# Kernel tuning notes

Hardware: AMD Instinct MI355X
Metric: run time of the kernel (lower is better)

Reference implementation:

```python
import jax, jax.numpy as jnp
import numpy as np
import math

DIM, DEPTH, HEADS, VOCAB, DMODEL = 200, 6, 10, 7, 512
DH = DIM // HEADS                      # 20
NBF = int(DH * math.log(DH))           # 59 FAVOR+ random features
FF = 4 * DIM                           # 800


def setup_inputs() -> dict:
    key = jax.random.key(0)
    ks = iter(jax.random.split(key, 32))
    s = 0.02
    inp = {
        'x': jax.random.normal(next(ks), (4, 16, 2048), jnp.float32),
        'token_emb': jax.random.normal(next(ks), (VOCAB, DIM)) * s,
        'ln1_g': jnp.ones((DEPTH, DIM)), 'ln1_b': jnp.zeros((DEPTH, DIM)),
        'wq': jax.random.normal(next(ks), (DEPTH, DIM, DIM)) * s, 'bq': jnp.zeros((DEPTH, DIM)),
        'wk': jax.random.normal(next(ks), (DEPTH, DIM, DIM)) * s, 'bk': jnp.zeros((DEPTH, DIM)),
        'wv': jax.random.normal(next(ks), (DEPTH, DIM, DIM)) * s, 'bv': jnp.zeros((DEPTH, DIM)),
        'proj': jax.random.normal(next(ks), (DEPTH, NBF, DH)),  # FAVOR+ projection (buffer)
        'wo': jax.random.normal(next(ks), (DEPTH, DIM, DIM)) * s, 'bo': jnp.zeros((DEPTH, DIM)),
        'ln2_g': jnp.ones((DEPTH, DIM)), 'ln2_b': jnp.zeros((DEPTH, DIM)),
        'ffw1': jax.random.normal(next(ks), (DEPTH, DIM, FF)) * s, 'ffb1': jnp.zeros((DEPTH, FF)),
        'ffw2': jax.random.normal(next(ks), (DEPTH, FF, DIM)) * s, 'ffb2': jnp.zeros((DEPTH, DIM)),
        'lnf_g': jnp.ones((DIM,)), 'lnf_b': jnp.zeros((DIM,)),
        'proj_w': jax.random.normal(next(ks), (DIM, DMODEL)) * s, 'proj_b': jnp.zeros((DMODEL,)),
    }
    return inp


def layer_norm(x, g, b, eps=1e-5):
    mu = x.mean(-1, keepdims=True)
    var = ((x - mu) ** 2).mean(-1, keepdims=True)
    return (x - mu) / jnp.sqrt(var + eps) * g + b


def softmax_kernel(data, proj, is_query, eps=1e-4):
    # data: (N,H,S,dh); proj: (m,dh)
    dn = data * (data.shape[-1] ** -0.25)
    dash = jnp.einsum('nhsd,md->nhsm', dn, proj)
    diag = 0.5 * jnp.sum(dn * dn, axis=-1, keepdims=True)
    mx = jnp.max(dash, axis=-1, keepdims=True) if is_query else jnp.max(dash)
    return (proj.shape[0] ** -0.5) * (jnp.exp(dash - diag - mx) + eps)


def attention(x, wq, bq, wk, bk, wv, bv, proj, wo, bo):
    N, S, D = x.shape
    split = lambda t: t.reshape(N, S, HEADS, DH).transpose(0, 2, 1, 3)
    q, k, v = split(x @ wq + bq), split(x @ wk + bk), split(x @ wv + bv)
    qp = softmax_kernel(q, proj, True)
    kp = softmax_kernel(k, proj, False)
    d_inv = 1.0 / jnp.einsum('nhsm,nhm->nhs', qp, kp.sum(axis=2))
    ctx = jnp.einsum('nhsm,nhsd->nhmd', kp, v)          # linear attention context
    out = jnp.einsum('nhsm,nhmd->nhsd', qp, ctx) * d_inv[..., None]
    return out.transpose(0, 2, 1, 3).reshape(N, S, D) @ wo + bo


def feedforward(x, w1, b1, w2, b2):
    return jax.nn.gelu(x @ w1 + b1, approximate=False) @ w2 + b2


def performer_forward(tokens, p):
    h = p['token_emb'][tokens]            # pos_emb is zeros (g2v_position_emb=False)
    x1, x2 = h, h                         # reversible net: x duplicated along channels
    for l in range(DEPTH):
        x1 = x1 + attention(layer_norm(x2, p['ln1_g'][l], p['ln1_b'][l]),
                            p['wq'][l], p['bq'][l], p['wk'][l], p['bk'][l],
                            p['wv'][l], p['bv'][l], p['proj'][l], p['wo'][l], p['bo'][l])
        x2 = x2 + feedforward(layer_norm(x1, p['ln2_g'][l], p['ln2_b'][l]),
                              p['ffw1'][l], p['ffb1'][l], p['ffw2'][l], p['ffb2'][l])
    h = 0.5 * (x1 + x2)                   # mean over the two reversible halves
    return layer_norm(h, p['lnf_g'], p['lnf_b'])


def reference(x, token_emb, ln1_g, ln1_b, wq, bq, wk, bk, wv, bv, proj, wo, bo,
              ln2_g, ln2_b, ffw1, ffb1, ffw2, ffb2, lnf_g, lnf_b, proj_w, proj_b):
    p = dict(token_emb=token_emb, ln1_g=ln1_g, ln1_b=ln1_b, wq=wq, bq=bq, wk=wk, bk=bk,
             wv=wv, bv=bv, proj=proj, wo=wo, bo=bo, ln2_g=ln2_g, ln2_b=ln2_b,
             ffw1=ffw1, ffb1=ffb1, ffw2=ffw2, ffb2=ffb2, lnf_g=lnf_g, lnf_b=lnf_b)
    B, Nt, T = x.shape
    xf = x.reshape(B * Nt, T)
    # torch.quantile on 1D positives -> bin_edges shape (1,4) != (T,4), so the
    # original falls back to zero bin edges; edges_plus = [0,0,0,0,inf], hence
    # token = 4 if value > 0 else 0, then + cls_token_id (1).
    tokens = jnp.where(xf > 0, 4, 0).astype(jnp.int32) + 1
    # chunk loop (chunk_size=512 samples) is identity math: run all at once
    enc = performer_forward(tokens, p)    # (B*Nt, T, DIM)
    pooled = enc.mean(axis=1)             # mean-pool over sequence
    out = pooled @ proj_w + proj_b
    return out.reshape(B, Nt, DMODEL)
```

## Files before the change

kernel.cpp:

```cpp
#include <hip/hip_runtime.h>
#include <hip/hip_bf16.h>
#include <math.h>

#define DEPTH   6
#define DIM     200
#define HEADS   10
#define DH      20
#define NBF     59
#define FFD     800
#define DMODEL  512
#define NSEQ    64
#define SEQ     2048
#define NTOK    (NSEQ*SEQ)
#define KPAD    224
#define BUFPAD  64
#define KNROW   40
#define VROW    136
#define KPROW   136
#define QPROW   72
#define CTXR    21
#define HSROW   132
#define HSTRIDE ((size_t)NTOK * DH)
#define PKV_E   (512*KPAD)
#define PQ_E    (256*KPAD)
#define PWO_E   (256*KPAD)
#define PF1_E   (896*KPAD)
#define PF2_E   (256*800)

typedef __hip_bfloat16 bf16;
typedef unsigned short u16;
typedef short s8v __attribute__((ext_vector_type(8)));
typedef short s4v __attribute__((ext_vector_type(4)));
typedef float f4v __attribute__((ext_vector_type(4)));

constexpr float SCALE = 0.4728708045015879f;
constexpr float RATIO = 0.1301889109808239f;
constexpr float KEPS  = 1e-4f;

__device__ __forceinline__ float b2f(bf16 v) { return __bfloat162float(v); }
__device__ __forceinline__ bf16 f2b(float v) { return __float2bfloat16(v); }
__device__ __forceinline__ float bfu(u16 u) {
    return __uint_as_float(((unsigned)u) << 16);
}
__device__ __forceinline__ u16 f2u(float v) {
    bf16 hb = __float2bfloat16(v);
    return *(u16*)&hb;
}
__device__ __forceinline__ float gelu_f(float x) {
    float inner = 0.7978845608028654f * (x + 0.044715f * x * x * x);
    float e = __expf(2.f * inner);
    return x * (1.f - 1.f / (e + 1.f));
}
__device__ __forceinline__ void gld_lds16(const short* g, short* l) {
    __builtin_amdgcn_global_load_lds(
        (const __attribute__((address_space(1))) void*)g,
        (__attribute__((address_space(3))) void*)l, 16, 0, 0);
}
#define MFMA16(a, b, c) __builtin_amdgcn_mfma_f32_16x16x32_bf16(a, b, c, 0, 0, 0)

__global__ void sentinel_kernel(float* out, float wsmb) {
    if (threadIdx.x == 0) out[0] = wsmb;
}

__global__ void zeropad_kernel(bf16* p1, bf16* p2, bf16* p3, bf16* p4) {
    int i = threadIdx.x;
    if (i < BUFPAD) {
        bf16 z = f2b(0.f);
        p1[i] = z; p2[i] = z; p3[i] = z; p4[i] = z;
    }
}

__global__ __launch_bounds__(256) void prep_layer(
        const float* __restrict__ wq, const float* __restrict__ wk,
        const float* __restrict__ wv, const float* __restrict__ wo,
        const float* __restrict__ f1, const float* __restrict__ f2,
        const float* __restrict__ g1, const float* __restrict__ b1,
        const float* __restrict__ g2, const float* __restrict__ b2,
        const float* __restrict__ bq, const float* __restrict__ bk,
        const float* __restrict__ bv, const float* __restrict__ f1b,
        bf16* __restrict__ pKV, bf16* __restrict__ pQ, bf16* __restrict__ pWO,
        bf16* __restrict__ pF1, bf16* __restrict__ pF2,
        float* __restrict__ uw) {
    int b = blockIdx.x, t = threadIdx.x;
    if (b < 448) {
        int idx = b * 256 + t;
        int row = idx / KPAD, k = idx % KPAD;
        float v = 0.f;
        if (k < DIM) {
            if (row < DIM) v = wk[(size_t)k * DIM + row] * g1[k];
            else if (row >= 256 && row < 256 + DIM)
                v = wv[(size_t)k * DIM + (row - 256)] * g1[k];
        }
        pKV[idx] = f2b(v);
    } else if (b < 672) {
        int idx = (b - 448) * 256 + t;
        int row = idx / KPAD, k = idx % KPAD;
        float v = (row < DIM && k < DIM) ? wq[(size_t)k * DIM + row] * g1[k] : 0.f;
        pQ[idx] = f2b(v);
    } else if (b < 896) {
        int idx = (b - 672) * 256 + t;
        int row = idx / KPAD, k = idx % KPAD;
        float v = (row < DIM && k < DIM) ? wo[(size_t)k * DIM + row] : 0.f;
        pWO[idx] = f2b(v);
    } else if (b < 1680) {
        int idx = (b - 896) * 256 + t;
        int row = idx / KPAD, k = idx % KPAD;
        float v = (row < FFD && k < DIM) ? f1[(size_t)k * FFD + row] * g2[k] : 0.f;
        pF1[idx] = f2b(v);
    } else if (b < 2480) {
        int idx = (b - 1680) * 256 + t;
        int row = idx / 800, k = idx % 800;
        float v = (row < DIM) ? f2[(size_t)k * DIM + row] : 0.f;
        pF2[idx] = f2b(v);
    } else if (b < 2482) {
        int j = b - 2480;
        const float* W    = j ? wv : wk;
        const float* bias = j ? bv : bk;
        int n = t;
        float su = 0.f, sw = 0.f;
        if (n < DIM) {
            for (int k = 0; k < DIM; ++k) {
                float wvv = W[(size_t)k * DIM + n];
                su += g1[k] * wvv;
                sw += b1[k] * wvv;
            }
            sw += bias[n];
        }
        uw[j * 256 + n] = su;
        uw[512 + j * 256 + n] = sw;
    } else if (b == 2482) {
        int n = t;
        float su = 0.f, sw = 0.f;
        if (n < DIM) {
            for (int k = 0; k < DIM; ++k) {
                float wvv = wq[(size_t)k * DIM + n];
                su += g1[k] * wvv;
                sw += b1[k] * wvv;
            }
            sw += bq[n];
        }
        uw[1024 + n] = su;
        uw[1280 + n] = sw;
    } else {
        int n = (b - 2483) * 256 + t;
        if (n < 896) {
            float su = 0.f, sw = 0.f;
            if (n < FFD) {
                for (int k = 0; k < DIM; ++k) {
                    float wvv = f1[(size_t)k * FFD + n];
                    su += g2[k] * wvv;
                    sw += b2[k] * wvv;
                }
                sw += f1b[n];
            }
            uw[1536 + n] = su;
            uw[2432 + n] = sw;
        }
    }
}

__global__ __launch_bounds__(256) void embed_kernel(const float* __restrict__ x,
        const float* __restrict__ emb, bf16* __restrict__ x1, bf16* __restrict__ x2) {
    int idx = blockIdx.x * 256 + threadIdx.x;
    if (idx >= NTOK * 25) return;
    int t = idx / 25, c = idx % 25;
    int row = (x[t] > 0.f) ? 5 : 1;
    const float4* e4 = (const float4*)(emb + row * DIM + c * 8);
    float4 e0 = e4[0], e1 = e4[1];
    s8v o;
    o[0] = (short)f2u(e0.x); o[1] = (short)f2u(e0.y);
    o[2] = (short)f2u(e0.z); o[3] = (short)f2u(e0.w);
    o[4] = (short)f2u(e1.x); o[5] = (short)f2u(e1.y);
    o[6] = (short)f2u(e1.z); o[7] = (short)f2u(e1.w);
    size_t off = (size_t)t * DIM + c * 8;
    *(s8v*)((short*)x1 + off) = o;
    *(s8v*)((short*)x2 + off) = o;
}

__global__ __launch_bounds__(256) void lnstats_kernel(const bf16* __restrict__ in,
        float* __restrict__ mu_o, float* __restrict__ rstd_o) {
    int lane = threadIdx.x & 63;
    size_t t = (size_t)blockIdx.x * 4 + (threadIdx.x >> 6);
    const u16* row = (const u16*)in + t * DIM;
    float v0 = 0.f, v1 = 0.f, v2 = 0.f, v3 = 0.f;
    if (lane < 50) {
        ushort4 u4 = ((const ushort4*)row)[lane];
        v0 = bfu(u4.x); v1 = bfu(u4.y); v2 = bfu(u4.z); v3 = bfu(u4.w);
    }
    float s = v0 + v1 + v2 + v3, qq = v0*v0 + v1*v1 + v2*v2 + v3*v3;
    #pragma unroll
    for (int o = 32; o > 0; o >>= 1) { s += __shfl_xor(s, o); qq += __shfl_xor(qq, o); }
    if (lane == 0) {
        float mu = s * (1.f / DIM);
        mu_o[t] = mu;
        rstd_o[t] = rsqrtf(qq * (1.f / DIM) - mu * mu + 1e-5f);
    }
}

__global__ __launch_bounds__(256) void finalln_kernel(const bf16* __restrict__ in1,
        const bf16* __restrict__ in2, const float* __restrict__ g,
        const float* __restrict__ b, bf16* __restrict__ out) {
    int lane = threadIdx.x & 63;
    size_t t = (size_t)blockIdx.x * 4 + (threadIdx.x >> 6);
    const u16* r1 = (const u16*)in1 + t * DIM;
    const u16* r2 = (const u16*)in2 + t * DIM;
    float v0 = 0.f, v1 = 0.f, v2 = 0.f, v3 = 0.f;
    if (lane < 50) {
        ushort4 a4 = ((const ushort4*)r1)[lane];
        ushort4 b4 = ((const ushort4*)r2)[lane];
        v0 = 0.5f * (bfu(a4.x) + bfu(b4.x));
        v1 = 0.5f * (bfu(a4.y) + bfu(b4.y));
        v2 = 0.5f * (bfu(a4.z) + bfu(b4.z));
        v3 = 0.5f * (bfu(a4.w) + bfu(b4.w));
    }
    float s = v0 + v1 + v2 + v3, qq = v0*v0 + v1*v1 + v2*v2 + v3*v3;
    #pragma unroll
    for (int o = 32; o > 0; o >>= 1) { s += __shfl_xor(s, o); qq += __shfl_xor(qq, o); }
    float mu = s * (1.f / DIM);
    float rstd = rsqrtf(qq * (1.f / DIM) - mu * mu + 1e-5f);
    if (lane < 50) {
        float4 g4 = ((const float4*)g)[lane];
        float4 b4f = ((const float4*)b)[lane];
        ushort4 o4;
        o4.x = f2u((v0 - mu) * rstd * g4.x + b4f.x);
        o4.y = f2u((v1 - mu) * rstd * g4.y + b4f.y);
        o4.z = f2u((v2 - mu) * rstd * g4.z + b4f.z);
        o4.w = f2u((v3 - mu) * rstd * g4.w + b4f.w);
        ((ushort4*)((u16*)out + t * DIM))[lane] = o4;
    }
}

template<int EPI, int LNE, int KV, int HB>
__global__ __launch_bounds__(256) void gemm_m(
        const bf16* __restrict__ A, const bf16* __restrict__ Bt,
        const float* __restrict__ wv_, const float* __restrict__ uv_,
        const float* __restrict__ mu, const float* __restrict__ rstd,
        bf16* __restrict__ C, bf16* __restrict__ C2,
        int M, int N, int K, int Kpad) {
    __shared__ __align__(16) short As[128 * 32];
    __shared__ __align__(16) short Bs[128 * 32];
    int bm = blockIdx.x * 128, bn = blockIdx.y * 128;
    int t = threadIdx.x, l = t & 63, w = t >> 6;
    int wr = (w >> 1) * 64, wc = (w & 1) * 64;
    int lr = l & 15, lk16 = l >> 4;
    f4v acc[4][4];
    #pragma unroll
    for (int i = 0; i < 4; ++i)
        #pragma unroll
        for (int j = 0; j < 4; ++j) acc[i][j] = (f4v){0.f, 0.f, 0.f, 0.f};

    const short* Ash = (const short*)A;
    const short* Bsh = (const short*)Bt;
    int srow0 = 32 * w + (l >> 2);
    int c16 = l & 3;
    for (int k0 = 0; k0 < Kpad; k0 += 32) {
        __syncthreads();
        #pragma unroll
        for (int j = 0; j < 2; ++j) {
            int row = srow0 + 16 * j;
            int xc = (c16 ^ ((row >> 1) & 3)) * 8;
            gld_lds16(Ash + (size_t)(bm + row) * K + k0 + xc,
                      &As[(32 * w + 16 * j) * 32]);
            gld_lds16(Bsh + (size_t)(bn + row) * Kpad + k0 + xc,
                      &Bs[(32 * w + 16 * j) * 32]);
        }
        __syncthreads();
        s8v a[4], b[4];
        #pragma unroll
        for (int fi = 0; fi < 4; ++fi) {
            int R = wr + fi * 16 + lr;
            a[fi] = *(const s8v*)&As[R * 32 + ((lk16 ^ ((R >> 1) & 3)) * 8)];
        }
        #pragma unroll
        for (int fj = 0; fj < 4; ++fj) {
            int R = wc + fj * 16 + lr;
            b[fj] = *(const s8v*)&Bs[R * 32 + ((lk16 ^ ((R >> 1) & 3)) * 8)];
        }
        #pragma unroll
        for (int fi = 0; fi < 4; ++fi)
            #pragma unroll
            for (int fj = 0; fj < 4; ++fj)
                acc[fi][fj] = MFMA16(a[fi], b[fj], acc[fi][fj]);
    }
    int r0 = (l >> 4) * 4;
    #pragma unroll
    for (int fi = 0; fi < 4; ++fi) {
        int rowb = bm + wr + fi * 16 + r0;
        float sr[4] = {1.f, 1.f, 1.f, 1.f}, tr[4] = {0.f, 0.f, 0.f, 0.f};
        if (LNE) {
            #pragma unroll
            for (int r = 0; r < 4; ++r) {
                sr[r] = rstd[rowb + r];
                tr[r] = mu[rowb + r] * sr[r];
            }
        }
        #pragma unroll
        for (int fj = 0; fj < 4; ++fj) {
            int col = bn + wc + fj * 16 + lr;
            if (KV) {
                int cc = col & 255;
                if (cc < DIM) {
                    bf16* dst = (col < 256) ? C : C2;
                    int hh = cc / DH, dd = cc % DH;
                    size_t base = (size_t)hh * HSTRIDE + dd;
                    float ww = wv_[col], uu = uv_[col];
                    #pragma unroll
                    for (int r = 0; r < 4; ++r) {
                        size_t idx = base + (size_t)(rowb + r) * DH;
                        float v = sr[r] * acc[fi][fj][r] - tr[r] * uu + ww;
                        dst[idx] = f2b(v);
                    }
                }
            } else if (col < N) {
                float ww = wv_[col];
                float uu = LNE ? uv_[col] : 0.f;
                #pragma unroll
                for (int r = 0; r < 4; ++r) {
                    size_t idx;
                    if (HB) {
                        int hh = col / DH, dd = col % DH;
                        idx = (size_t)hh * HSTRIDE + (size_t)(rowb + r) * DH + dd;
                    } else {
                        idx = (size_t)(rowb + r) * N + col;
                    }
                    float v = LNE ? (sr[r] * acc[fi][fj][r] - tr[r] * uu + ww)
                                  : (acc[fi][fj][r] + ww);
                    if (EPI == 1) v += b2f(C[idx]);
                    if (EPI == 2) v = gelu_f(v);
                    C[idx] = f2b(v);
                }
            }
        }
    }
}

__global__ __launch_bounds__(256, 2) void ff_fused(
        const bf16* __restrict__ x1, const bf16* __restrict__ pF1,
        const bf16* __restrict__ pF2, const float* __restrict__ u1,
        const float* __restrict__ w1f, const float* __restrict__ fb2,
        const float* __restrict__ mu_in, const float* __restrict__ rstd_in,
        float* __restrict__ mu_out, float* __restrict__ rstd_out,
        bf16* __restrict__ x2) {
    __shared__ __align__(16) short Ax[64 * 256];
    __shared__ __align__(16) short Bs[2 * 128 * 32];
    __shared__ __align__(16) short hS[64 * HSROW];
    int bm = blockIdx.x * 64;
    int t = threadIdx.x, l = t & 63, w = t >> 6;
    int wrA = (w >> 1) * 32;
    int wcA = (w & 1) * 64;
    int wcB = (w & 1) * 128;
    int lr = l & 15, lk16 = l >> 4;
    int r0 = (l >> 4) * 4;
    const short* X1 = (const short*)x1;
    const short* F1 = (const short*)pF1;
    const short* F2 = (const short*)pF2;

    {
        int c = l & 31, rsub = l >> 5;
        #pragma unroll
        for (int j = 0; j < 8; ++j) {
            int row0 = w * 16 + j * 2;
            int row = row0 + rsub;
            gld_lds16(X1 + (size_t)(bm + row) * DIM + ((c ^ (row & 7)) * 8),
                      &Ax[row0 * 256]);
        }
    }

    f4v acc2[2][8];
    #pragma unroll
    for (int i = 0; i < 2; ++i)
        #pragma unroll
        for (int j = 0; j < 8; ++j) acc2[i][j] = (f4v){0.f, 0.f, 0.f, 0.f};

    int srow0 = 32 * w + (l >> 2);
    int c16 = l & 3;
    #pragma unroll 1
    for (int hc = 0; hc < 7; ++hc) {
        __syncthreads();
        #pragma unroll
        for (int j = 0; j < 2; ++j) {
            int row = srow0 + 16 * j;
            int xc = (c16 ^ ((row >> 1) & 3)) * 8;
            gld_lds16(F1 + (size_t)(hc * 128 + row) * KPAD + 0 + xc,
                      &Bs[(32 * w + 16 * j) * 32]);
        }
        __syncthreads();
        f4v acc1[2][4];
        #pragma unroll
        for (int i = 0; i < 2; ++i)
            #pragma unroll
            for (int j = 0; j < 4; ++j) acc1[i][j] = (f4v){0.f, 0.f, 0.f, 0.f};
        #pragma unroll 1
        for (int kt = 0; kt < 7; ++kt) {
            if (kt < 6) {
                int k0n = (kt + 1) * 32;
                int hb = ((kt + 1) & 1) * 4096;
                #pragma unroll
                for (int j = 0; j < 2; ++j) {
                    int row = srow0 + 16 * j;
                    int xc = (c16 ^ ((row >> 1) & 3)) * 8;
                    gld_lds16(F1 + (size_t)(hc * 128 + row) * KPAD + k0n + xc,
                              &Bs[hb + (32 * w + 16 * j) * 32]);
                }
            }
            int hb = (kt & 1) * 4096;
            s8v a[2], b[4];
            int cg = kt * 4 + lk16;
            #pragma unroll
            for (int fi = 0; fi < 2; ++fi) {
                int R = wrA + fi * 16 + lr;
                a[fi] = *(const s8v*)&Ax[R * 256 + ((cg ^ (R & 7)) * 8)];
            }
            #pragma unroll
            for (int fj = 0; fj < 4; ++fj) {
                int R = wcA + fj * 16 + lr;
                b[fj] = *(const s8v*)&Bs[hb + R * 32 + ((lk16 ^ ((R >> 1) & 3)) * 8)];
            }
            #pragma unroll
            for (int fi = 0; fi < 2; ++fi)
                #pragma unroll
                for (int fj = 0; fj < 4; ++fj)
                    acc1[fi][fj] = MFMA16(a[fi], b[fj], acc1[fi][fj]);
            __syncthreads();
        }
        #pragma unroll
        for (int j = 0; j < 4; ++j) {
            int row = (w * 4 + j) * 16 + (l >> 2);
            int xc = (c16 ^ ((row >> 1) & 3)) * 8;
            gld_lds16(F2 + (size_t)row * 800 + hc * 128 + 0 + xc,
                      &Bs[(w * 4 + j) * 16 * 32]);
        }
        #pragma unroll
        for (int fi = 0; fi < 2; ++fi) {
            int rowL = wrA + fi * 16 + r0;
            f4v rs = *(const f4v*)&rstd_in[bm + rowL];
            f4v mm = *(const f4v*)&mu_in[bm + rowL];
            #pragma unroll
            for (int fj = 0; fj < 4; ++fj) {
                int col = wcA + fj * 16 + lr;
                int gcol = hc * 128 + col;
                float uu = u1[gcol], ww = w1f[gcol];
                #pragma unroll
                for (int r = 0; r < 4; ++r) {
                    float v = rs[r] * acc1[fi][fj][r] - mm[r] * rs[r] * uu + ww;
                    v = gelu_f(v);
                    int rr = rowL + r;
                    hS[rr * HSROW + (((col >> 3) ^ (rr & 7)) * 8) + (col & 7)]
                        = (short)f2u(v);
                }
            }
        }
        #pragma unroll 1
        for (int ks = 0; ks < 4; ++ks) {
            if (ks) {
                __syncthreads();
                #pragma unroll
                for (int j = 0; j < 4; ++j) {
                    int row = (w * 4 + j) * 16 + (l >> 2);
                    int xc = (c16 ^ ((row >> 1) & 3)) * 8;
                    gld_lds16(F2 + (size_t)row * 800 + hc * 128 + ks * 32 + xc,
                              &Bs[(w * 4 + j) * 16 * 32]);
                }
            }
            __syncthreads();
            s8v a[2];
            int cg = ks * 4 + lk16;
            #pragma unroll
            for (int fi = 0; fi < 2; ++fi) {
                int R = wrA + fi * 16 + lr;
                a[fi] = *(const s8v*)&hS[R * HSROW + ((cg ^ (R & 7)) * 8)];
            }
            #pragma unroll
            for (int fj = 0; fj < 8; ++fj) {
                int Br = wcB + fj * 16 + lr;
                s8v bfr = *(const s8v*)&Bs[Br * 32 + ((lk16 ^ ((Br >> 1) & 3)) * 8)];
                #pragma unroll
                for (int fi = 0; fi < 2; ++fi)
                    acc2[fi][fj] = MFMA16(a[fi], bfr, acc2[fi][fj]);
            }
        }
    }
    __syncthreads();
    float* sp = (float*)hS;
    float rsum[2][4], rsq[2][4];
    #pragma unroll
    for (int fi = 0; fi < 2; ++fi)
        #pragma unroll
        for (int r = 0; r < 4; ++r) { rsum[fi][r] = 0.f; rsq[fi][r] = 0.f; }
    #pragma unroll
    for (int fi = 0; fi < 2; ++fi) {
        int rowb = bm + wrA + fi * 16 + r0;
        #pragma unroll
        for (int fj = 0; fj < 8; ++fj) {
            int col = wcB + fj * 16 + lr;
            if (col < DIM) {
                float bb = fb2[col];
                #pragma unroll
                for (int r = 0; r < 4; ++r) {
                    size_t idx = (size_t)(rowb + r) * DIM + col;
                    float v = acc2[fi][fj][r] + bb + b2f(x2[idx]);
                    x2[idx] = f2b(v);
                    rsum[fi][r] += v;
                    rsq[fi][r] += v * v;
                }
            }
        }
    }
    #pragma unroll
    for (int fi = 0; fi < 2; ++fi)
        #pragma unroll
        for (int r = 0; r < 4; ++r) {
            float s = rsum[fi][r], q = rsq[fi][r];
            #pragma unroll
            for (int o = 8; o > 0; o >>= 1) {
                s += __shfl_xor(s, o);
                q += __shfl_xor(q, o);
            }
            rsum[fi][r] = s; rsq[fi][r] = q;
        }
    if (lr == 0) {
        #pragma unroll
        for (int fi = 0; fi < 2; ++fi)
            #pragma unroll
            for (int r = 0; r < 4; ++r) {
                int rowL = wrA + fi * 16 + r0 + r;
                sp[rowL * 4 + (w & 1) * 2 + 0] = rsum[fi][r];
                sp[rowL * 4 + (w & 1) * 2 + 1] = rsq[fi][r];
            }
    }
    __syncthreads();
    if (t < 64) {
        float s = sp[t * 4 + 0] + sp[t * 4 + 2];
        float q = sp[t * 4 + 1] + sp[t * 4 + 3];
        float mu = s * (1.f / DIM);
        mu_out[bm + t] = mu;
        rstd_out[bm + t] = rsqrtf(q * (1.f / DIM) - mu * mu + 1e-5f);
    }
}

__global__ __launch_bounds__(256) void kvctx_mfma(const bf16* __restrict__ k,
        const bf16* __restrict__ v, const float* __restrict__ proj,
        float* __restrict__ ctxg) {
    __shared__ __align__(16) short ph[64 * KNROW];
    __shared__ __align__(16) short pl[64 * KNROW];
    __shared__ __align__(16) short knh[128 * KNROW];
    __shared__ __align__(16) short knl[128 * KNROW];
    __shared__ __align__(16) short vT[32 * VROW];
    __shared__ __align__(16) short kp[64 * KPROW];
    __shared__ __align__(16) float diag[128];
    __shared__ float wmax[4];
    int nh = blockIdx.x, n = nh / HEADS, h = nh % HEADS;
    int t = threadIdx.x, l = t & 63, w = t >> 6;
    int lr = l & 15, lk = (l >> 4) * 8, l4 = (l >> 4) * 4;
    const u16* kbase = (const u16*)k + (size_t)h * HSTRIDE;
    const u16* vbase = (const u16*)v + (size_t)h * HSTRIDE;
    for (int i = t; i < 64 * 32; i += 256) {
        int m = i >> 5, d = i & 31;
        float val = (m < NBF && d < DH) ? proj[m * DH + d] : 0.f;
        u16 hi = f2u(val);
        ph[m * KNROW + d] = (short)hi;
        pl[m * KNROW + d] = (short)f2u(val - bfu(hi));
    }
    for (int i = t; i < 128 * 12; i += 256) {
        int s = i / 12, d = 20 + i % 12;
        knh[s * KNROW + d] = 0; knl[s * KNROW + d] = 0;
    }
    for (int i = t; i < 12 * 128; i += 256) {
        int d = 20 + (i >> 7), s = i & 127;
        vT[d * VROW + s] = (short)((d == 20) ? f2u(1.0f) : 0);
    }
    s8v ones;
    #pragma unroll
    for (int i = 0; i < 8; ++i) ones[i] = (short)f2u(1.0f);
    float Mrun = -3.0e38f;
    f4v cd0 = {0.f,0.f,0.f,0.f}, cd1 = {0.f,0.f,0.f,0.f};
    f4v vs0 = {0.f,0.f,0.f,0.f}, vs1 = {0.f,0.f,0.f,0.f};
    for (int c = 0; c < 16; ++c) {
        int s0 = c * 128;
        __syncthreads();
        if (t < 128) {
            int s = t;
            const u16* kr = kbase + (size_t)(n * SEQ + s0 + s) * DH;
            float dg = 0.f;
            #pragma unroll
            for (int q5 = 0; q5 < 5; ++q5) {
                ushort4 u4 = ((const ushort4*)kr)[q5];
                float f0 = bfu(u4.x) * SCALE, f1 = bfu(u4.y) * SCALE;
                float f2_ = bfu(u4.z) * SCALE, f3 = bfu(u4.w) * SCALE;
                dg += f0*f0 + f1*f1 + f2_*f2_ + f3*f3;
                u16 h0 = f2u(f0), h1 = f2u(f1), h2 = f2u(f2_), h3 = f2u(f3);
                s4v hv = {(short)h0, (short)h1, (short)h2, (short)h3};
                *(s4v*)&knh[s * KNROW + q5 * 4] = hv;
                s4v lv = {(short)f2u(f0 - bfu(h0)), (short)f2u(f1 - bfu(h1)),
                          (short)f2u(f2_ - bfu(h2)), (short)f2u(f3 - bfu(h3))};
                *(s4v*)&knl[s * KNROW + q5 * 4] = lv;
            }
            diag[s] = 0.5f * dg;
        } else {
            int s = t - 128;
            const u16* vr = vbase + (size_t)(n * SEQ + s0 + s) * DH;
            #pragma unroll
            for (int q5 = 0; q5 < 5; ++q5) {
                ushort4 u4 = ((const ushort4*)vr)[q5];
                vT[(q5 * 4 + 0) * VROW + s] = (short)u4.x;
                vT[(q5 * 4 + 1) * VROW + s] = (short)u4.y;
                vT[(q5 * 4 + 2) * VROW + s] = (short)u4.z;
                vT[(q5 * 4 + 3) * VROW + s] = (short)u4.w;
            }
        }
        __syncthreads();
        s8v ah0 = *(const s8v*)&knh[(32 * w + lr) * KNROW + lk];
        s8v al0 = *(const s8v*)&knl[(32 * w + lr) * KNROW + lk];
        s8v ah1 = *(const s8v*)&knh[(32 * w + 16 + lr) * KNROW + lk];
        s8v al1 = *(const s8v*)&knl[(32 * w + 16 + lr) * KNROW + lk];
        f4v dg0 = *(const f4v*)&diag[32 * w + l4];
        f4v dg1 = *(const f4v*)&diag[32 * w + 16 + l4];
        f4v D0[4], D1[4];
        #pragma unroll
        for (int mt = 0; mt < 4; ++mt) {
            s8v bh = *(const s8v*)&ph[(mt * 16 + lr) * KNROW + lk];
            s8v bl = *(const s8v*)&pl[(mt * 16 + lr) * KNROW + lk];
            f4v d0 = {0.f, 0.f, 0.f, 0.f}, d1 = {0.f, 0.f, 0.f, 0.f};
            d0 = MFMA16(ah0, bh, d0); d0 = MFMA16(ah0, bl, d0); d0 = MFMA16(al0, bh, d0);
            d1 = MFMA16(ah1, bh, d1); d1 = MFMA16(ah1, bl, d1); d1 = MFMA16(al1, bh, d1);
            D0[mt] = d0; D1[mt] = d1;
        }
        float mm = -3.0e38f;
        #pragma unroll
        for (int mt = 0; mt < 4; ++mt) {
            int lim = (mt < 3) ? 16 : (NBF - 48);
            if (lr < lim) {
                #pragma unroll
                for (int r = 0; r < 4; ++r)
                    mm = fmaxf(mm, fmaxf(D0[mt][r], D1[mt][r]));
            }
        }
        #pragma unroll
        for (int o = 32; o > 0; o >>= 1) mm = fmaxf(mm, __shfl_xor(mm, o));
        if (l == 0) wmax[w] = mm;
        __syncthreads();
        float Mnew = fmaxf(fmaxf(wmax[0], wmax[1]), fmaxf(wmax[2], wmax[3]));
        Mnew = fmaxf(Mrun, Mnew);
        float scl = __expf(Mrun - Mnew);
        #pragma unroll
        for (int r = 0; r < 4; ++r) { cd0[r] *= scl; cd1[r] *= scl; }
        Mrun = Mnew;
        #pragma unroll
        for (int mt = 0; mt < 4; ++mt) {
            int m = mt * 16 + lr;
            bool valid = m < NBF;
            s4v o0, o1;
            #pragma unroll
            for (int r = 0; r < 4; ++r) {
                float kp0 = valid ? __expf(D0[mt][r] - dg0[r] - Mnew) : 0.f;
                float kp1 = valid ? __expf(D1[mt][r] - dg1[r] - Mnew) : 0.f;
                o0[r] = (short)f2u(kp0);
                o1[r] = (short)f2u(kp1);
            }
            *(s4v*)&kp[m * KPROW + 32 * w + l4] = o0;
            *(s4v*)&kp[m * KPROW + 32 * w + 16 + l4] = o1;
        }
        __syncthreads();
        #pragma unroll
        for (int ks = 0; ks < 4; ++ks) {
            s8v a  = *(const s8v*)&kp[(16 * w + lr) * KPROW + ks * 32 + lk];
            s8v b0 = *(const s8v*)&vT[lr * VROW + ks * 32 + lk];
            s8v b1 = *(const s8v*)&vT[(16 + lr) * VROW + ks * 32 + lk];
            cd0 = MFMA16(a, b0, cd0);
            cd1 = MFMA16(a, b1, cd1);
            vs0 = MFMA16(ones, b0, vs0);
            vs1 = MFMA16(ones, b1, vs1);
        }
    }
    float* cg = ctxg + (size_t)nh * CTXR * 64;
    int m0 = 16 * w + l4;
    f4v r0v, r1v;
    #pragma unroll
    for (int r = 0; r < 4; ++r) {
        r0v[r] = RATIO * (cd0[r] + KEPS * vs0[r]);
        r1v[r] = RATIO * (cd1[r] + KEPS * vs1[r]);
    }
    *(f4v*)&cg[lr * 64 + m0] = r0v;
    if (lr < 5) *(f4v*)&cg[(16 + lr) * 64 + m0] = r1v;
}

__global__ __launch_bounds__(256) void qattn_mfma(const bf16* __restrict__ q,
        const float* __restrict__ proj, const float* __restrict__ ctxg,
        bf16* __restrict__ ao) {
    __shared__ __align__(16) short ph[64 * KNROW];
    __shared__ __align__(16) short pl[64 * KNROW];
    __shared__ __align__(16) short qnh[128 * KNROW];
    __shared__ __align__(16) short qnl[128 * KNROW];
    __shared__ __align__(16) short qp[128 * QPROW];
    __shared__ __align__(16) short cT[32 * QPROW];
    __shared__ __align__(16) float dgs[128];
    __shared__ __align__(16) float osf[128][22];
    int b = blockIdx.x;
    int nh = b >> 2, sc = b & 3;
    int n = nh / HEADS, h = nh % HEADS;
    int t = threadIdx.x, l = t & 63, w = t >> 6;
    int lr = l & 15, lk = (l >> 4) * 8, l4 = (l >> 4) * 4;
    const u16* qbase = (const u16*)q + (size_t)h * HSTRIDE;
    for (int i = t; i < 64 * 32; i += 256) {
        int m = i >> 5, d = i & 31;
        float val = (m < NBF && d < DH) ? proj[m * DH + d] : 0.f;
        u16 hi = f2u(val);
        ph[m * KNROW + d] = (short)hi;
        pl[m * KNROW + d] = (short)f2u(val - bfu(hi));
    }
    for (int i = t; i < 128 * 12; i += 256) {
        int s = i / 12, d = 20 + i % 12;
        qnh[s * KNROW + d] = 0; qnl[s * KNROW + d] = 0;
    }
    for (int i = t; i < 32 * 64; i += 256) {
        int d = i >> 6, m = i & 63;
        float val = (d < CTXR) ? ctxg[(size_t)nh * CTXR * 64 + d * 64 + m] : 0.f;
        cT[d * QPROW + m] = (short)f2u(val);
    }
    for (int c = 0; c < 4; ++c) {
        int s0 = (sc * 4 + c) * 128;
        __syncthreads();
        if (t < 128) {
            int s = t;
            const u16* qr = qbase + (size_t)(n * SEQ + s0 + s) * DH;
            float dg = 0.f;
            #pragma unroll
            for (int q5 = 0; q5 < 5; ++q5) {
                ushort4 u4 = ((const ushort4*)qr)[q5];
                float f0 = bfu(u4.x) * SCALE, f1 = bfu(u4.y) * SCALE;
                float f2_ = bfu(u4.z) * SCALE, f3 = bfu(u4.w) * SCALE;
                dg += f0*f0 + f1*f1 + f2_*f2_ + f3*f3;
                u16 h0 = f2u(f0), h1 = f2u(f1), h2 = f2u(f2_), h3 = f2u(f3);
                s4v hv = {(short)h0, (short)h1, (short)h2, (short)h3};
                *(s4v*)&qnh[s * KNROW + q5 * 4] = hv;
                s4v lv = {(short)f2u(f0 - bfu(h0)), (short)f2u(f1 - bfu(h1)),
                          (short)f2u(f2_ - bfu(h2)), (short)f2u(f3 - bfu(h3))};
                *(s4v*)&qnl[s * KNROW + q5 * 4] = lv;
            }
            dgs[s] = 0.5f * dg;
        }
        __syncthreads();
        s8v ah0 = *(const s8v*)&qnh[(32 * w + lr) * KNROW + lk];
        s8v al0 = *(const s8v*)&qnl[(32 * w + lr) * KNROW + lk];
        s8v ah1 = *(const s8v*)&qnh[(32 * w + 16 + lr) * KNROW + lk];
        s8v al1 = *(const s8v*)&qnl[(32 * w + 16 + lr) * KNROW + lk];
        f4v D0[4], D1[4];
        #pragma unroll
        for (int mt = 0; mt < 4; ++mt) {
            s8v bh = *(const s8v*)&ph[(mt * 16 + lr) * KNROW + lk];
            s8v bl = *(const s8v*)&pl[(mt * 16 + lr) * KNROW + lk];
            f4v d0 = {0.f, 0.f, 0.f, 0.f}, d1 = {0.f, 0.f, 0.f, 0.f};
            d0 = MFMA16(ah0, bh, d0); d0 = MFMA16(ah0, bl, d0); d0 = MFMA16(al0, bh, d0);
            d1 = MFMA16(ah1, bh, d1); d1 = MFMA16(ah1, bl, d1); d1 = MFMA16(al1, bh, d1);
            D0[mt] = d0; D1[mt] = d1;
        }
        f4v dg0 = *(const f4v*)&dgs[32 * w + l4];
        f4v dg1 = *(const f4v*)&dgs[32 * w + 16 + l4];
        float mx0[4], mx1[4];
        #pragma unroll
        for (int r = 0; r < 4; ++r) {
            float v3 = (lr < NBF - 48) ? D0[3][r] : -3.4e38f;
            float mm = fmaxf(fmaxf(D0[0][r], D0[1][r]), fmaxf(D0[2][r], v3));
            mm = fmaxf(mm, __shfl_xor(mm, 1));
            mm = fmaxf(mm, __shfl_xor(mm, 2));
            mm = fmaxf(mm, __shfl_xor(mm, 4));
            mm = fmaxf(mm, __shfl_xor(mm, 8));
            mx0[r] = mm;
            float u3 = (lr < NBF - 48) ? D1[3][r] : -3.4e38f;
            float nn = fmaxf(fmaxf(D1[0][r], D1[1][r]), fmaxf(D1[2][r], u3));
            nn = fmaxf(nn, __shfl_xor(nn, 1));
            nn = fmaxf(nn, __shfl_xor(nn, 2));
            nn = fmaxf(nn, __shfl_xor(nn, 4));
            nn = fmaxf(nn, __shfl_xor(nn, 8));
            mx1[r] = nn;
        }
        #pragma unroll
        for (int mt = 0; mt < 4; ++mt) {
            int m = mt * 16 + lr;
            bool valid = m < NBF;
            #pragma unroll
            for (int r = 0; r < 4; ++r) {
                float p0 = valid ? RATIO * (__expf(D0[mt][r] - dg0[r] - mx0[r]) + KEPS) : 0.f;
                float p1 = valid ? RATIO * (__expf(D1[mt][r] - dg1[r] - mx1[r]) + KEPS) : 0.f;
                qp[(32 * w + l4 + r) * QPROW + m] = (short)f2u(p0);
                qp[(32 * w + 16 + l4 + r) * QPROW + m] = (short)f2u(p1);
            }
        }
        __syncthreads();
        f4v o00 = {0.f,0.f,0.f,0.f}, o01 = {0.f,0.f,0.f,0.f};
        f4v o10 = {0.f,0.f,0.f,0.f}, o11 = {0.f,0.f,0.f,0.f};
        #pragma unroll
        for (int ks = 0; ks < 2; ++ks) {
            s8v a0 = *(const s8v*)&qp[(32 * w + lr) * QPROW + ks * 32 + lk];
            s8v a1 = *(const s8v*)&qp[(32 * w + 16 + lr) * QPROW + ks * 32 + lk];
            s8v b0 = *(const s8v*)&cT[lr * QPROW + ks * 32 + lk];
            s8v b1 = *(const s8v*)&cT[(16 + lr) * QPROW + ks * 32 + lk];
            o00 = MFMA16(a0, b0, o00); o01 = MFMA16(a0, b1, o01);
            o10 = MFMA16(a1, b0, o10); o11 = MFMA16(a1, b1, o11);
        }
        #pragma unroll
        for (int r = 0; r < 4; ++r) {
            osf[32 * w + l4 + r][lr] = o00[r];
            osf[32 * w + 16 + l4 + r][lr] = o10[r];
            if (lr < 5) {
                osf[32 * w + l4 + r][16 + lr] = o01[r];
                osf[32 * w + 16 + l4 + r][16 + lr] = o11[r];
            }
        }
        __syncthreads();
        if (t < 128) osf[t][21] = 1.f / osf[t][20];
        __syncthreads();
        int tokb = n * SEQ + s0;
        for (int idx = t; idx < 128 * 10; idx += 256) {
            int row = idx / 10, seg = idx % 10;
            float di = osf[row][21];
            ushort2 o2;
            o2.x = f2u(osf[row][seg * 2] * di);
            o2.y = f2u(osf[row][seg * 2 + 1] * di);
            *(ushort2*)((u16*)ao + (size_t)(tokb + row) * DIM + h * DH + seg * 2) = o2;
        }
    }
}

__global__ __launch_bounds__(256) void pool1_kernel(const bf16* __restrict__ hn,
        float* __restrict__ partial) {
    int n = blockIdx.x / 16, c = blockIdx.x % 16;
    int d = threadIdx.x;
    if (d >= DIM) return;
    float acc = 0.f;
    const bf16* base = hn + ((size_t)n * SEQ + c * 128) * DIM + d;
    for (int s = 0; s < 128; ++s) acc += b2f(base[(size_t)s * DIM]);
    partial[(size_t)blockIdx.x * DIM + d] = acc;
}

__global__ __launch_bounds__(256) void pool2_kernel(const float* __restrict__ partial,
        float* __restrict__ pooled) {
    int n = blockIdx.x, d = threadIdx.x;
    if (d >= DIM) return;
    float acc = 0.f;
    for (int c = 0; c < 16; ++c) acc += partial[(size_t)(n * 16 + c) * DIM + d];
    pooled[n * DIM + d] = acc * (1.f / SEQ);
}

__global__ __launch_bounds__(512) void finalproj_kernel(const float* __restrict__ pooled,
        const float* __restrict__ pw, const float* __restrict__ pb,
        float* __restrict__ out) {
    __shared__ float ps[DIM];
    int n = blockIdx.x;
    for (int i = threadIdx.x; i < DIM; i += 512) ps[i] = pooled[n * DIM + i];
    __syncthreads();
    int j = threadIdx.x;
    float acc = pb[j];
    for (int d = 0; d < DIM; ++d) acc += ps[d] * pw[d * DMODEL + j];
    out[n * DMODEL + j] = acc;
}

extern "C" void kernel_launch(void* const* d_in, const int* in_sizes, int n_in,
                              void* d_out, int out_size, void* d_ws, size_t ws_size,
                              hipStream_t stream) {
    (void)in_sizes; (void)n_in; (void)out_size;
    const float* x    = (const float*)d_in[0];
    const float* emb  = (const float*)d_in[1];
    const float* ln1g = (const float*)d_in[2];
    const float* ln1b = (const float*)d_in[3];
    const float* wq   = (const float*)d_in[4];
    const float* bq   = (const float*)d_in[5];
    const float* wk   = (const float*)d_in[6];
    const float* bk   = (const float*)d_in[7];
    const float* wv   = (const float*)d_in[8];
    const float* bv   = (const float*)d_in[9];
    const float* proj = (const float*)d_in[10];
    const float* wo   = (const float*)d_in[11];
    const float* bo   = (const float*)d_in[12];
    const float* ln2g = (const float*)d_in[13];
    const float* ln2b = (const float*)d_in[14];
    const float* ffw1 = (const float*)d_in[15];
    const float* ffb1 = (const float*)d_in[16];
    const float* ffw2 = (const float*)d_in[17];
    const float* ffb2 = (const float*)d_in[18];
    const float* lnfg = (const float*)d_in[19];
    const float* lnfb = (const float*)d_in[20];
    const float* pw   = (const float*)d_in[21];
    const float* pb   = (const float*)d_in[22];
    float* out = (float*)d_out;

    const size_t A_ = (size_t)NTOK * DIM;
    bf16* x1 = (bf16*)d_ws;
    bf16* x2 = x1 + A_ + BUFPAD;
    bf16* b3 = x2 + A_ + BUFPAD;
    bf16* b4 = b3 + A_ + BUFPAD;
    bf16* pKV = b4 + A_ + BUFPAD;
    bf16* pQ  = pKV + PKV_E;
    bf16* pWO = pQ + PQ_E;
    bf16* pF1 = pWO + PWO_E;
    bf16* pF2 = pF1 + PF1_E;
    float* muB   = (float*)(pF2 + PF2_E);
    float* rstdB = muB + NTOK;
    float* muC   = rstdB + NTOK;
    float* rstdC = muC + NTOK;
    float* uw    = rstdC + NTOK;
    float* ctxg  = uw + 3328;
    float* wsend = ctxg + (size_t)NSEQ * HEADS * CTXR * 64;

    float* ukv = uw,        *wkv = uw + 512;
    float* uq  = uw + 1024, *wqf = uw + 1280;
    float* u1  = uw + 1536, *w1f = uw + 2432;

    size_t need = (char*)wsend - (char*)d_ws;
    if (ws_size < need) {
        sentinel_kernel<<<1, 64, 0, stream>>>(out, (float)(ws_size >> 20));
        return;
    }

    zeropad_kernel<<<1, 64, 0, stream>>>(x1 + A_, x2 + A_, b3 + A_, b4 + A_);
    embed_kernel<<<(NTOK * 25 + 255) / 256, 256, 0, stream>>>(x, emb, x1, x2);
    lnstats_kernel<<<NTOK / 4, 256, 0, stream>>>(x2, muB, rstdB);

    dim3 gkv(NTOK / 128, 4);
    dim3 gd(NTOK / 128, 2);
    for (int l = 0; l < DEPTH; ++l) {
        const float* wq_l = wq + (size_t)l * DIM * DIM;
        const float* wk_l = wk + (size_t)l * DIM * DIM;
        const float* wv_l = wv + (size_t)l * DIM * DIM;
        const float* wo_l = wo + (size_t)l * DIM * DIM;
        const float* f1_l = ffw1 + (size_t)l * DIM * FFD;
        const float* f2_l = ffw2 + (size_t)l * FFD * DIM;
        const float* pj_l = proj + (size_t)l * NBF * DH;
        const float* g1 = ln1g + l * DIM, *b1 = ln1b + l * DIM;
        const float* g2 = ln2g + l * DIM, *b2 = ln2b + l * DIM;

        prep_layer<<<2487, 256, 0, stream>>>(wq_l, wk_l, wv_l, wo_l, f1_l, f2_l,
                g1, b1, g2, b2, bq + l * DIM, bk + l * DIM, bv + l * DIM,
                ffb1 + l * FFD, pKV, pQ, pWO, pF1, pF2, uw);

        gemm_m<0, 1, 1, 0><<<gkv, 256, 0, stream>>>(x2, pKV, wkv, ukv, muB, rstdB,
                b3, b4, NTOK, 512, DIM, KPAD);
        kvctx_mfma<<<NSEQ * HEADS, 256, 0, stream>>>(b3, b4, pj_l, ctxg);
        gemm_m<0, 1, 0, 1><<<gd, 256, 0, stream>>>(x2, pQ, wqf, uq, muB, rstdB,
                b3, nullptr, NTOK, DIM, DIM, KPAD);
        qattn_mfma<<<NSEQ * HEADS * 4, 256, 0, stream>>>(b3, pj_l, ctxg, b4);
        gemm_m<1, 0, 0, 0><<<gd, 256, 0, stream>>>(b4, pWO, bo + l * DIM, nullptr,
                nullptr, nullptr, x1, nullptr, NTOK, DIM, DIM, KPAD);

        lnstats_kernel<<<NTOK / 4, 256, 0, stream>>>(x1, muC, rstdC);
        ff_fused<<<NTOK / 64, 256, 0, stream>>>(x1, pF1, pF2, u1, w1f,
                ffb2 + l * DIM, muC, rstdC, muB, rstdB, x2);
    }

    finalln_kernel<<<NTOK / 4, 256, 0, stream>>>(x1, x2, lnfg, lnfb, b3);
    float* partial = muB;
    float* pooled  = muB + (size_t)NSEQ * 16 * DIM;
    pool1_kernel<<<NSEQ * 16, 256, 0, stream>>>(b3, partial);
    pool2_kernel<<<NSEQ, 256, 0, stream>>>(partial, pooled);
    finalproj_kernel<<<NSEQ, 512, 0, stream>>>(pooled, pw, pb, out);
}
```

Measured before the change: 4.198 ms.

## Replace tiled GEMMs with row-block fused kernels and fold LN stats into WO

Replaces the generic 128x128 gemm_m with a mat_fused kernel in which each block loads a 64-row strip of the activation (all K) into LDS once. It then loops over every output column chunk, streaming weight panels with double buffering. The WO projection kernel now accumulates per-row sum and sum-of-squares while adding the residual and writes the LayerNorm mean/rstd itself, so the separate lnstats launch before the feed-forward is dropped. The trade-offs are higher LDS use per block and fewer, longer blocks in exchange for avoiding repeated A reads and one full pass over x1.

```diff
diff --git a/kernel.cpp b/kernel.cpp
--- a/kernel.cpp
+++ b/kernel.cpp
@@ -230,106 +230,179 @@
     }
 }
 
-template<int EPI, int LNE, int KV, int HB>
-__global__ __launch_bounds__(256) void gemm_m(
-        const bf16* __restrict__ A, const bf16* __restrict__ Bt,
-        const float* __restrict__ wv_, const float* __restrict__ uv_,
-        const float* __restrict__ mu, const float* __restrict__ rstd,
-        bf16* __restrict__ C, bf16* __restrict__ C2,
-        int M, int N, int K, int Kpad) {
-    __shared__ __align__(16) short As[128 * 32];
-    __shared__ __align__(16) short Bs[128 * 32];
-    int bm = blockIdx.x * 128, bn = blockIdx.y * 128;
+template<int MODE>
+__global__ __launch_bounds__(256, 2) void mat_fused(
+        const bf16* __restrict__ A, const bf16* __restrict__ panel,
+        const float* __restrict__ uvec, const float* __restrict__ wvec,
+        const float* __restrict__ mu_in, const float* __restrict__ rstd_in,
+        bf16* __restrict__ dst0, bf16* __restrict__ dst1,
+        float* __restrict__ mu_out, float* __restrict__ rstd_out) {
+    constexpr int NCH = (MODE == 0) ? 4 : 2;
+    __shared__ __align__(16) short Ax[64 * 256];
+    __shared__ __align__(16) short Bs[2 * 128 * 32];
+    int bm = blockIdx.x * 64;
     int t = threadIdx.x, l = t & 63, w = t >> 6;
-    int wr = (w >> 1) * 64, wc = (w & 1) * 64;
+    int wrA = (w >> 1) * 32;
+    int wcA = (w & 1) * 64;
     int lr = l & 15, lk16 = l >> 4;
-    f4v acc[4][4];
+    int r0 = (l >> 4) * 4;
+    const short* Ash = (const short*)A;
+    const short* P = (const short*)panel;
+
+    {
+        int c = l & 31, rsub = l >> 5;
+        #pragma unroll
+        for (int j = 0; j < 8; ++j) {
+            int row0 = w * 16 + j * 2;
+            int row = row0 + rsub;
+            gld_lds16(Ash + (size_t)(bm + row) * DIM + ((c ^ (row & 7)) * 8),
+                      &Ax[row0 * 256]);
+        }
+    }
+
+    float rsum[2][4], rsq[2][4];
     #pragma unroll
-    for (int i = 0; i < 4; ++i)
-        #pragma unroll
-        for (int j = 0; j < 4; ++j) acc[i][j] = (f4v){0.f, 0.f, 0.f, 0.f};
-
-    const short* Ash = (const short*)A;
-    const short* Bsh = (const short*)Bt;
+    for (int fi = 0; fi < 2; ++fi)
+        #pragma unroll
+        for (int r = 0; r < 4; ++r) { rsum[fi][r] = 0.f; rsq[fi][r] = 0.f; }
+
     int srow0 = 32 * w + (l >> 2);
     int c16 = l & 3;
-    for (int k0 = 0; k0 < Kpad; k0 += 32) {
+    #pragma unroll 1
+    for (int ch = 0; ch < NCH; ++ch) {
         __syncthreads();
         #pragma unroll
         for (int j = 0; j < 2; ++j) {
             int row = srow0 + 16 * j;
             int xc = (c16 ^ ((row >> 1) & 3)) * 8;
-            gld_lds16(Ash + (size_t)(bm + row) * K + k0 + xc,
-                      &As[(32 * w + 16 * j) * 32]);
-            gld_lds16(Bsh + (size_t)(bn + row) * Kpad + k0 + xc,
+            gld_lds16(P + (size_t)(ch * 128 + row) * KPAD + 0 + xc,
                       &Bs[(32 * w + 16 * j) * 32]);
         }
         __syncthreads();
-        s8v a[4], b[4];
-        #pragma unroll
-        for (int fi = 0; fi < 4; ++fi) {
-            int R = wr + fi * 16 + lr;
-            a[fi] = *(const s8v*)&As[R * 32 + ((lk16 ^ ((R >> 1) & 3)) * 8)];
-        }
-        #pragma unroll
-        for (int fj = 0; fj < 4; ++fj) {
-            int R = wc + fj * 16 + lr;
-            b[fj] = *(const s8v*)&Bs[R * 32 + ((lk16 ^ ((R >> 1) & 3)) * 8)];
-        }
-        #pragma unroll
-        for (int fi = 0; fi < 4; ++fi)
-            #pragma unroll
-            for (int fj = 0; fj < 4; ++fj)
-                acc[fi][fj] = MFMA16(a[fi], b[fj], acc[fi][fj]);
-    }
-    int r0 = (l >> 4) * 4;
-    #pragma unroll
-    for (int fi = 0; fi < 4; ++fi) {
-        int rowb = bm + wr + fi * 16 + r0;
-        float sr[4] = {1.f, 1.f, 1.f, 1.f}, tr[4] = {0.f, 0.f, 0.f, 0.f};
-        if (LNE) {
-            #pragma unroll
-            for (int r = 0; r < 4; ++r) {
-                sr[r] = rstd[rowb + r];
-                tr[r] = mu[rowb + r] * sr[r];
-            }
-        }
-        #pragma unroll
-        for (int fj = 0; fj < 4; ++fj) {
-            int col = bn + wc + fj * 16 + lr;
-            if (KV) {
-                int cc = col & 255;
-                if (cc < DIM) {
-                    bf16* dst = (col < 256) ? C : C2;
-                    int hh = cc / DH, dd = cc % DH;
-                    size_t base = (size_t)hh * HSTRIDE + dd;
-                    float ww = wv_[col], uu = uv_[col];
-                    #pragma unroll
-                    for (int r = 0; r < 4; ++r) {
-                        size_t idx = base + (size_t)(rowb + r) * DH;
-                        float v = sr[r] * acc[fi][fj][r] - tr[r] * uu + ww;
-                        dst[idx] = f2b(v);
+        f4v acc1[2][4];
+        #pragma unroll
+        for (int i = 0; i < 2; ++i)
+            #pragma unroll
+            for (int j = 0; j < 4; ++j) acc1[i][j] = (f4v){0.f, 0.f, 0.f, 0.f};
+        #pragma unroll 1
+        for (int kt = 0; kt < 7; ++kt) {
+            if (kt < 6) {
+                int k0n = (kt + 1) * 32;
+                int hb = ((kt + 1) & 1) * 4096;
+                #pragma unroll
+                for (int j = 0; j < 2; ++j) {
+                    int row = srow0 + 16 * j;
+                    int xc = (c16 ^ ((row >> 1) & 3)) * 8;
+                    gld_lds16(P + (size_t)(ch * 128 + row) * KPAD + k0n + xc,
+                              &Bs[hb + (32 * w + 16 * j) * 32]);
+                }
+            }
+            int hb = (kt & 1) * 4096;
+            s8v a[2], b[4];
+            int cg = kt * 4 + lk16;
+            #pragma unroll
+            for (int fi = 0; fi < 2; ++fi) {
+                int R = wrA + fi * 16 + lr;
+                a[fi] = *(const s8v*)&Ax[R * 256 + ((cg ^ (R & 7)) * 8)];
+            }
+            #pragma unroll
+            for (int fj = 0; fj < 4; ++fj) {
+                int R = wcA + fj * 16 + lr;
+                b[fj] = *(const s8v*)&Bs[hb + R * 32 + ((lk16 ^ ((R >> 1) & 3)) * 8)];
+            }
+            #pragma unroll
+            for (int fi = 0; fi < 2; ++fi)
+                #pragma unroll
+                for (int fj = 0; fj < 4; ++fj)
+                    acc1[fi][fj] = MFMA16(a[fi], b[fj], acc1[fi][fj]);
+            __syncthreads();
+        }
+        #pragma unroll
+        for (int fi = 0; fi < 2; ++fi) {
+            int rowb = bm + wrA + fi * 16 + r0;
+            f4v rs, mm;
+            if (MODE != 2) {
+                rs = *(const f4v*)&rstd_in[rowb];
+                mm = *(const f4v*)&mu_in[rowb];
+            }
+            #pragma unroll
+            for (int fj = 0; fj < 4; ++fj) {
+                int col = ch * 128 + wcA + fj * 16 + lr;
+                if (MODE == 0) {
+                    int cc = col & 255;
+                    if (cc < DIM) {
+                        bf16* dst = (col < 256) ? dst0 : dst1;
+                        int hh = cc / DH, dd = cc % DH;
+                        float ww = wvec[col], uu = uvec[col];
+                        #pragma unroll
+                        for (int r = 0; r < 4; ++r) {
+                            size_t idx = (size_t)hh * HSTRIDE
+                                       + (size_t)(rowb + r) * DH + dd;
+                            float v = rs[r] * acc1[fi][fj][r]
+                                    - mm[r] * rs[r] * uu + ww;
+                            dst[idx] = f2b(v);
+                        }
+                    }
+                } else if (MODE == 1) {
+                    if (col < DIM) {
+                        int hh = col / DH, dd = col % DH;
+                        float ww = wvec[col], uu = uvec[col];
+                        #pragma unroll
+                        for (int r = 0; r < 4; ++r) {
+                            size_t idx = (size_t)hh * HSTRIDE
+                                       + (size_t)(rowb + r) * DH + dd;
+                            float v = rs[r] * acc1[fi][fj][r]
+                                    - mm[r] * rs[r] * uu + ww;
+                            dst0[idx] = f2b(v);
+                        }
+                    }
+                } else {
+                    if (col < DIM) {
+                        float bb = wvec[col];
+                        #pragma unroll
+                        for (int r = 0; r < 4; ++r) {
+                            size_t idx = (size_t)(rowb + r) * DIM + col;
+                            float v = acc1[fi][fj][r] + bb + b2f(dst0[idx]);
+                            dst0[idx] = f2b(v);
+                            rsum[fi][r] += v;
+                            rsq[fi][r] += v * v;
+                        }
                     }
                 }
-            } else if (col < N) {
-                float ww = wv_[col];
-                float uu = LNE ? uv_[col] : 0.f;
+            }
+        }
+    }
+    if (MODE == 2) {
+        #pragma unroll
+        for (int fi = 0; fi < 2; ++fi)
+            #pragma unroll
+            for (int r = 0; r < 4; ++r) {
+                float s = rsum[fi][r], q = rsq[fi][r];
+                #pragma unroll
+                for (int o = 8; o > 0; o >>= 1) {
+                    s += __shfl_xor(s, o);
+                    q += __shfl_xor(q, o);
+                }
+                rsum[fi][r] = s; rsq[fi][r] = q;
+            }
+        float* sp = (float*)Bs;
+        if (lr == 0) {
+            #pragma unroll
+            for (int fi = 0; fi < 2; ++fi)
                 #pragma unroll
                 for (int r = 0; r < 4; ++r) {
-                    size_t idx;
-                    if (HB) {
-                        int hh = col / DH, dd = col % DH;
-                        idx = (size_t)hh * HSTRIDE + (size_t)(rowb + r) * DH + dd;
-                    } else {
-                        idx = (size_t)(rowb + r) * N + col;
-                    }
-                    float v = LNE ? (sr[r] * acc[fi][fj][r] - tr[r] * uu + ww)
-                                  : (acc[fi][fj][r] + ww);
-                    if (EPI == 1) v += b2f(C[idx]);
-                    if (EPI == 2) v = gelu_f(v);
-                    C[idx] = f2b(v);
+                    int rowL = wrA + fi * 16 + r0 + r;
+                    sp[rowL * 4 + (w & 1) * 2 + 0] = rsum[fi][r];
+                    sp[rowL * 4 + (w & 1) * 2 + 1] = rsq[fi][r];
                 }
-            }
+        }
+        __syncthreads();
+        if (t < 64) {
+            float s = sp[t * 4 + 0] + sp[t * 4 + 2];
+            float q = sp[t * 4 + 1] + sp[t * 4 + 3];
+            float mu = s * (1.f / DIM);
+            mu_out[bm + t] = mu;
+            rstd_out[bm + t] = rsqrtf(q * (1.f / DIM) - mu * mu + 1e-5f);
         }
     }
 }
@@ -916,8 +989,6 @@
     embed_kernel<<<(NTOK * 25 + 255) / 256, 256, 0, stream>>>(x, emb, x1, x2);
     lnstats_kernel<<<NTOK / 4, 256, 0, stream>>>(x2, muB, rstdB);
 
-    dim3 gkv(NTOK / 128, 4);
-    dim3 gd(NTOK / 128, 2);
     for (int l = 0; l < DEPTH; ++l) {
         const float* wq_l = wq + (size_t)l * DIM * DIM;
         const float* wk_l = wk + (size_t)l * DIM * DIM;
@@ -933,16 +1004,15 @@
                 g1, b1, g2, b2, bq + l * DIM, bk + l * DIM, bv + l * DIM,
                 ffb1 + l * FFD, pKV, pQ, pWO, pF1, pF2, uw);
 
-        gemm_m<0, 1, 1, 0><<<gkv, 256, 0, stream>>>(x2, pKV, wkv, ukv, muB, rstdB,
-                b3, b4, NTOK, 512, DIM, KPAD);
+        mat_fused<0><<<NTOK / 64, 256, 0, stream>>>(x2, pKV, ukv, wkv,
+                muB, rstdB, b3, b4, nullptr, nullptr);
         kvctx_mfma<<<NSEQ * HEADS, 256, 0, stream>>>(b3, b4, pj_l, ctxg);
-        gemm_m<0, 1, 0, 1><<<gd, 256, 0, stream>>>(x2, pQ, wqf, uq, muB, rstdB,
-                b3, nullptr, NTOK, DIM, DIM, KPAD);
+        mat_fused<1><<<NTOK / 64, 256, 0, stream>>>(x2, pQ, uq, wqf,
+                muB, rstdB, b3, nullptr, nullptr, nullptr);
         qattn_mfma<<<NSEQ * HEADS * 4, 256, 0, stream>>>(b3, pj_l, ctxg, b4);
-        gemm_m<1, 0, 0, 0><<<gd, 256, 0, stream>>>(b4, pWO, bo + l * DIM, nullptr,
-                nullptr, nullptr, x1, nullptr, NTOK, DIM, DIM, KPAD);
-
-        lnstats_kernel<<<NTOK / 4, 256, 0, stream>>>(x1, muC, rstdC);
+        mat_fused<2><<<NTOK / 64, 256, 0, stream>>>(b4, pWO, nullptr, bo + l * DIM,
+                nullptr, nullptr, x1, nullptr, muC, rstdC);
+
         ff_fused<<<NTOK / 64, 256, 0, stream>>>(x1, pF1, pF2, u1, w1f,
                 ffb2 + l * DIM, muC, rstdC, muB, rstdB, x2);
     }
```

New measurement: 3.856 ms. -8.2%, faster.
